# Kernel tuning notes

Hardware: AMD Instinct MI355X
Metric: run time of the kernel (lower is better)

## Reference

```python
import jax, jax.numpy as jnp
import numpy as np

# dims
T, INPUT_DIM = 128, 512
C_INT, ISQ, DIM, C = 8, 16, 256, 8  # internal_channels, input_square_dim, dim, n_channel
OSQ, OUT_CH = 8, 16                  # output_square_dim, output_size // osq^2
INPUT_SCALE, S1, S2 = 1.0, 0.9, 0.1
K1, D1, K2, D2 = 3, 1, 5, 2


def dw_circ_conv(x, w, dilation):
    """Depthwise conv with circular padding. x: [B,C,H,W], w: [C,1,k,k]."""
    k = w.shape[-1]
    pad = dilation * (k - 1) // 2
    xp = jnp.pad(x, ((0, 0), (0, 0), (pad, pad), (pad, pad)), mode='wrap')
    return jax.lax.conv_general_dilated(
        xp, w, window_strides=(1, 1), padding='VALID',
        rhs_dilation=(dilation, dilation), feature_group_count=x.shape[1])


def setup_inputs() -> dict:
    key = jax.random.key(0)
    ks = jax.random.split(key, 10)
    X = jax.random.normal(ks[0], (T, INPUT_DIM), jnp.float32)
    # nn.Linear weight [out, in]
    W_embed = jax.random.normal(ks[1], (C_INT * ISQ * ISQ, INPUT_DIM), jnp.float32) * 0.02
    mask_coarse = jax.random.bernoulli(ks[2], 0.5, (1, 1, ISQ, ISQ)).astype(jnp.float32)
    mask_fine = jax.random.bernoulli(ks[3], 0.5, (1, 1, DIM, DIM)).astype(jnp.float32)
    # ConvTranspose2d weight [in_ch, out_ch, k, k], k = dim // isq = 16
    W_deconv = jax.random.normal(ks[4], (C_INT, C, DIM // ISQ, DIM // ISQ), jnp.float32) * 0.02

    def lateral_w(k, ksz, p):
        # LateralConnections with conn_exp=1: |w| * bernoulli(p), normalized per output channel
        w = jnp.abs(jax.random.normal(k, (C, 1, ksz, ksz), jnp.float32))
        m = jax.random.bernoulli(jax.random.fold_in(k, 1), p, w.shape).astype(jnp.float32)
        w = w * m
        return w / w.sum(axis=(1, 2, 3), keepdims=True)

    w1 = lateral_w(ks[5], K1, 0.9)
    w2 = lateral_w(ks[6], K2, 0.9)
    # output Conv2d: [out_ch, in_ch, k, k], k = dim // osq = 32
    w_out = jax.random.normal(ks[7], (OUT_CH, C, DIM // OSQ, DIM // OSQ), jnp.float32) * 0.01
    b_out = jax.random.normal(ks[8], (OUT_CH,), jnp.float32) * 0.01
    return dict(X=X, W_embed=W_embed, mask_coarse=mask_coarse, mask_fine=mask_fine,
                W_deconv=W_deconv, w1=w1, w2=w2, w_out=w_out, b_out=b_out)


def reference(X, W_embed, mask_coarse, mask_fine, W_deconv, w1, w2, w_out, b_out):
    t = X.shape[0]
    ksz = W_deconv.shape[-1]
    # CorticalInput
    u = (X @ W_embed.T).reshape(t, C_INT, ISQ, ISQ) * mask_coarse  # [T,Cint,isq,isq]
    # ConvTranspose2d with stride == kernel_size (non-overlapping) == block expansion
    u = jnp.einsum('tcij,coab->toiajb', u, W_deconv).reshape(t, C, ISQ * ksz, ISQ * ksz)
    u = INPUT_SCALE * u * mask_fine  # [T,C,dim,dim]

    # sequential reservoir scan
    def step(Z, x):
        Z = jnp.tanh(S1 * dw_circ_conv(Z, w1, D1) + S2 * dw_circ_conv(Z, w2, D2) + x)
        return Z, Z[0]

    Z0 = jnp.zeros((1, C, DIM, DIM), X.dtype)
    _, outs = jax.lax.scan(step, Z0, u)  # outs: [T,C,dim,dim]

    # readout conv (kernel == stride == dim // osq)
    ko = w_out.shape[-1]
    y = jax.lax.conv_general_dilated(outs, w_out, (ko, ko), 'VALID')
    y = y + b_out[None, :, None, None]
    return y.reshape(t, -1)
```

## Files before the change

### kernel.cpp

```cpp
#include <hip/hip_runtime.h>
#include <math.h>

#define SB_OFF   0
#define E_OFF    1048576
#define YP_OFF   1310720

__device__ __forceinline__ float fast_tanh(float x) {
  x = fminf(fmaxf(x, -15.f), 15.f);
  float ex = __expf(2.f * x);
  return __fdividef(ex - 1.f, ex + 1.f);
}

template <int CTRL>
__device__ __forceinline__ float dpp_add(float v) {
  int x = __builtin_amdgcn_update_dpp(0, __float_as_int(v), CTRL, 0xF, 0xF, true);
  return v + __int_as_float(x);
}

__device__ __forceinline__ float2 aload_f2(const float* p) {
  unsigned long long v = __hip_atomic_load((const unsigned long long*)p,
                                           __ATOMIC_RELAXED, __HIP_MEMORY_SCOPE_AGENT);
  float2 r;
  r.x = __uint_as_float((unsigned)v);
  r.y = __uint_as_float((unsigned)(v >> 32));
  return r;
}
__device__ __forceinline__ void astore_f2(float* p, float a, float b) {
  unsigned long long v =
      ((unsigned long long)__float_as_uint(b) << 32) | (unsigned long long)__float_as_uint(a);
  __hip_atomic_store((unsigned long long*)p, v, __ATOMIC_RELAXED, __HIP_MEMORY_SCOPE_AGENT);
}

__global__ __launch_bounds__(256) void prep_kernel(
    const float* __restrict__ X, const float* __restrict__ W_embed,
    const float* __restrict__ mask_coarse, float* __restrict__ ws)
{
  const int tid = threadIdx.x, bid = blockIdx.x;
  float* eb = ws + E_OFF;
  const int o  = bid * 8 + (tid >> 5);
  const int t0 = (tid & 31) * 4;
  const float4* Wf4 = (const float4*)W_embed + (size_t)o * 128;
  const float4* Xf4 = (const float4*)X;
  float acc[4] = {0.f, 0.f, 0.f, 0.f};
  for (int k4 = 0; k4 < 128; ++k4) {
    float4 wv = Wf4[k4];
#pragma unroll
    for (int tt = 0; tt < 4; ++tt) {
      float4 xv = Xf4[(size_t)(t0 + tt) * 128 + k4];
      acc[tt] = fmaf(wv.x, xv.x, fmaf(wv.y, xv.y, fmaf(wv.z, xv.z, fmaf(wv.w, xv.w, acc[tt]))));
    }
  }
  float mc = mask_coarse[o & 255];
#pragma unroll
  for (int tt = 0; tt < 4; ++tt)
    eb[(size_t)(t0 + tt) * 2048 + o] = acc[tt] * mc;
}

__global__ __launch_bounds__(512, 2) void scan_kernel(
    const float* __restrict__ mask_fine, const float* __restrict__ W_deconv,
    const float* __restrict__ w1, const float* __restrict__ w2,
    const float* __restrict__ w_out, float* __restrict__ ws)
{
  __shared__ float zin[72 * 44];
  __shared__ float rowbuf[64 * 19];

  const int tid  = threadIdx.x;
  const int bid  = blockIdx.x;
  const int ch   = bid >> 5;
  const int tile = bid & 31;
  const int tI = tile >> 3, tJ = tile & 7;
  const int r0 = tI << 6, c0 = tJ << 5;
  const int row = tid >> 3;
  const int cg  = tid & 7;
  const int lc  = cg << 2;

  float* Zb = ws + SB_OFF;
  const float* eb = ws + E_OFF;
  float* yp = ws + YP_OFF;
  const int myoff = (ch * 32 + tile) << 11;

  const int a16 = row & 15;
  const int b16 = lc & 15;
  const int i0  = (r0 + row) >> 4;
  const int jj  = (c0 + lc) >> 4;
  float4 wd[8];
#pragma unroll
  for (int c = 0; c < 8; ++c)
    wd[c] = *(const float4*)&W_deconv[(((c * 8 + ch) * 16) + a16) * 16 + b16];
  float4 mf = *(const float4*)&mask_fine[(size_t)(r0 + row) * 256 + c0 + lc];
  float4 wo[16];
#pragma unroll
  for (int oc = 0; oc < 16; ++oc)
    wo[oc] = *(const float4*)&w_out[(((oc * 8 + ch) * 32) + (row & 31)) * 32 + lc];
  float w1s[9], w2s[25];
#pragma unroll
  for (int k = 0; k < 9; ++k)
    w1s[k] = __uint_as_float(__builtin_amdgcn_readfirstlane(__float_as_uint(w1[ch * 9 + k])));
#pragma unroll
  for (int k = 0; k < 25; ++k)
    w2s[k] = __uint_as_float(__builtin_amdgcn_readfirstlane(__float_as_uint(w2[ch * 25 + k])));

  int rd_off[2] = {0, 0}, rd_dst[2] = {0, 0};
  {
    int n = 0;
    auto setup = [&](int u) {
      int di = 0, dj = 0, off = 0, dst = 0;
      if (u < 128) {
        int r = u >> 5, c = u & 31;
        di = -1; dj = 0; off = 256 + 2 * u; dst = r * 44 + 4 + c;
      } else if (u < 256) {
        int v = u - 128;
        di = 1; dj = 0; off = 2 * v; dst = (68 + (v >> 5)) * 44 + 4 + (v & 31);
      } else if (u < 512) {
        int v = u - 256;
        di = 0; dj = -1; off = 1024 + 2 * v; dst = (4 + (v >> 2)) * 44 + (v & 3);
      } else if (u < 768) {
        int v = u - 512;
        di = 0; dj = 1; off = 512 + 2 * v; dst = (4 + (v >> 2)) * 44 + 36 + (v & 3);
      } else {
        int v = u - 768; int corner = v >> 4, k = v & 15, r = k >> 2, c = k & 3;
        if (corner == 0)      { di = -1; dj = -1; off = 1632 + 2 * k; dst = r * 44 + c; }
        else if (corner == 1) { di = -1; dj = 1;  off = 1600 + 2 * k; dst = r * 44 + 36 + c; }
        else if (corner == 2) { di = 1;  dj = -1; off = 1568 + 2 * k; dst = (68 + r) * 44 + c; }
        else                  { di = 1;  dj = 1;  off = 1536 + 2 * k; dst = (68 + r) * 44 + 36 + c; }
      }
      int nI = (tI + di) & 3, nJ = (tJ + dj) & 7;
      rd_off[n] = ((ch * 32 + nI * 8 + nJ) << 11) + off;
      rd_dst[n] = dst;
      ++n;
    };
    setup(tid);
    if (tid < 320) setup(tid + 512);
  }
  const bool has2 = (tid < 320);

  for (int k = tid; k < 72 * 44; k += 512) zin[k] = 0.f;
  __syncthreads();

  for (int t = 0; t < 128; ++t) {
    float* sb = Zb + (size_t)((t + 1) & 1) * 524288;

    float ev[8];
#pragma unroll
    for (int c = 0; c < 8; ++c)
      ev[c] = eb[(size_t)t * 2048 + c * 256 + i0 * 16 + jj];

    float c1a[4] = {0, 0, 0, 0}, c2a[4] = {0, 0, 0, 0};
    {
      float w[12];
      auto load_row = [&](int zr) {
        float4 A  = *(const float4*)&zin[zr * 44 + lc];
        float4 B  = *(const float4*)&zin[zr * 44 + lc + 4];
        float4 Cq = *(const float4*)&zin[zr * 44 + lc + 8];
        w[0]=A.x; w[1]=A.y; w[2]=A.z; w[3]=A.w;
        w[4]=B.x; w[5]=B.y; w[6]=B.z; w[7]=B.w;
        w[8]=Cq.x; w[9]=Cq.y; w[10]=Cq.z; w[11]=Cq.w;
      };
      auto k2row = [&](int a) {
#pragma unroll
        for (int j = 0; j < 4; ++j)
#pragma unroll
          for (int b = 0; b < 5; ++b)
            c2a[j] = fmaf(w[j + 2 * b], w2s[a * 5 + b], c2a[j]);
      };
      auto k1row = [&](int a) {
#pragma unroll
        for (int j = 0; j < 4; ++j)
#pragma unroll
          for (int b = 0; b < 3; ++b)
            c1a[j] = fmaf(w[j + 3 + b], w1s[a * 3 + b], c1a[j]);
      };
      load_row(row + 0); k2row(0);
      load_row(row + 2); k2row(1);
      load_row(row + 3); k1row(0);
      load_row(row + 4); k1row(1); k2row(2);
      load_row(row + 5); k1row(2);
      load_row(row + 6); k2row(3);
      load_row(row + 8); k2row(4);
    }
    float zv[4];
    {
      const float* mfp = (const float*)&mf;
#pragma unroll
      for (int j = 0; j < 4; ++j) {
        float u = 0.f;
#pragma unroll
        for (int c = 0; c < 8; ++c)
          u = fmaf(ev[c], ((const float*)&wd[c])[j], u);
        float val = fmaf(0.9f, c1a[j], fmaf(0.1f, c2a[j], mfp[j] * u));
        zv[j] = fast_tanh(val);
      }
    }

    if (t < 127) {
      float* myrec = sb + myoff;
      const float tagf = __uint_as_float((unsigned)(t + 1));
      if (row < 4) {
#pragma unroll
        for (int j = 0; j < 4; ++j)
          astore_f2(myrec + 2 * (row * 32 + lc + j), zv[j], tagf);
      }
      if (row >= 60) {
#pragma unroll
        for (int j = 0; j < 4; ++j)
          astore_f2(myrec + 256 + 2 * ((row - 60) * 32 + lc + j), zv[j], tagf);
      }
      if (lc == 0) {
#pragma unroll
        for (int j = 0; j < 4; ++j)
          astore_f2(myrec + 512 + 2 * (row * 4 + j), zv[j], tagf);
      }
      if (lc == 28) {
#pragma unroll
        for (int j = 0; j < 4; ++j)
          astore_f2(myrec + 1024 + 2 * (row * 4 + j), zv[j], tagf);
      }
      if (row < 4 && lc == 0) {
#pragma unroll
        for (int j = 0; j < 4; ++j)
          astore_f2(myrec + 1536 + 2 * (row * 4 + j), zv[j], tagf);
      }
      if (row < 4 && lc == 28) {
#pragma unroll
        for (int j = 0; j < 4; ++j)
          astore_f2(myrec + 1568 + 2 * (row * 4 + j), zv[j], tagf);
      }
      if (row >= 60 && lc == 0) {
#pragma unroll
        for (int j = 0; j < 4; ++j)
          astore_f2(myrec + 1600 + 2 * ((row - 60) * 4 + j), zv[j], tagf);
      }
      if (row >= 60 && lc == 28) {
#pragma unroll
        for (int j = 0; j < 4; ++j)
          astore_f2(myrec + 1632 + 2 * ((row - 60) * 4 + j), zv[j], tagf);
      }
    }

    float racc[16];
#pragma unroll
    for (int oc = 0; oc < 16; ++oc) {
      const float* wop = (const float*)&wo[oc];
      racc[oc] = fmaf(zv[0], wop[0], fmaf(zv[1], wop[1], fmaf(zv[2], wop[2], zv[3] * wop[3])));
    }

    __syncthreads();

    *(float4*)&zin[(4 + row) * 44 + 4 + lc] = make_float4(zv[0], zv[1], zv[2], zv[3]);

#pragma unroll
    for (int k = 0; k < 16; ++k) {
      racc[k] = dpp_add<0xB1>(racc[k]);
      racc[k] = dpp_add<0x4E>(racc[k]);
      racc[k] = dpp_add<0x141>(racc[k]);
    }
    rowbuf[row * 19 + (cg << 1)]     = racc[cg << 1];
    rowbuf[row * 19 + (cg << 1) + 1] = racc[(cg << 1) + 1];

    if (t < 127) {
      const unsigned tg = (unsigned)(t + 1);
      {
        const float* p = sb + rd_off[0];
        float2 v2; int spins = 0;
        do { v2 = aload_f2(p);
             if (__float_as_uint(v2.y) == tg) break;
             __builtin_amdgcn_s_sleep(1);
        } while (++spins < (1 << 17));
        zin[rd_dst[0]] = v2.x;
      }
      if (has2) {
        const float* p = sb + rd_off[1];
        float2 v2; int spins = 0;
        do { v2 = aload_f2(p);
             if (__float_as_uint(v2.y) == tg) break;
             __builtin_amdgcn_s_sleep(1);
        } while (++spins < (1 << 17));
        zin[rd_dst[1]] = v2.x;
      }
    }

    __syncthreads();

    if (tid < 32) {
      int p = tid >> 4, oc = tid & 15;
      float s = 0.f;
#pragma unroll
      for (int r = 0; r < 32; ++r) s += rowbuf[(p * 32 + r) * 19 + oc];
      yp[(((size_t)ch * 64 + (2 * tI + p) * 8 + tJ) * 128 + t) * 16 + oc] = s;
    }
  }
}

__global__ __launch_bounds__(256) void final_kernel(
    const float* __restrict__ b_out, const float* __restrict__ ws, float* __restrict__ out)
{
  int idx = blockIdx.x * 256 + threadIdx.x;
  int t = idx >> 10;
  int rem = idx & 1023;
  int oc = rem >> 6;
  int IJ = rem & 63;
  const float* yp = ws + YP_OFF;
  float s = b_out[oc];
#pragma unroll
  for (int c = 0; c < 8; ++c)
    s += yp[(((size_t)c * 64 + IJ) * 128 + t) * 16 + oc];
  out[idx] = s;
}

extern "C" void kernel_launch(void* const* d_in, const int* in_sizes, int n_in,
                              void* d_out, int out_size, void* d_ws, size_t ws_size,
                              hipStream_t stream) {
  const float* X           = (const float*)d_in[0];
  const float* W_embed     = (const float*)d_in[1];
  const float* mask_coarse = (const float*)d_in[2];
  const float* mask_fine   = (const float*)d_in[3];
  const float* W_deconv    = (const float*)d_in[4];
  const float* w1          = (const float*)d_in[5];
  const float* w2          = (const float*)d_in[6];
  const float* w_out       = (const float*)d_in[7];
  const float* b_out       = (const float*)d_in[8];
  float* ws  = (float*)d_ws;
  float* out = (float*)d_out;

  prep_kernel<<<dim3(256), dim3(256), 0, stream>>>(X, W_embed, mask_coarse, ws);
  scan_kernel<<<dim3(256), dim3(512), 0, stream>>>(mask_fine, W_deconv, w1, w2, w_out, ws);
  final_kernel<<<dim3(512), dim3(256), 0, stream>>>(b_out, ws, out);
}
```

Baseline: 555.8 us.

## Split scan into 512 smaller tiles and fuse readout reduction via atomics

Halves the spatial tile per block (32x32 instead of 64x32), doubling the grid to 512 blocks of 256 threads so more CUs take part in the sequential scan, with halo exchange records resized accordingly. The separate final reduction kernel is removed: prep initializes the output with the bias, and each scan block atomically adds its per-channel readout partial sums directly into the output. The smaller tiles mean more halo traffic per element and more inter-block spin synchronization. The atomic accumulation changes summation order, and all 512 blocks must be co-resident for the spin-wait scheme to work.

```diff
diff --git a/kernel.cpp b/kernel.cpp
--- a/kernel.cpp
+++ b/kernel.cpp
@@ -2,8 +2,7 @@
 #include <math.h>
 
 #define SB_OFF   0
-#define E_OFF    1048576
-#define YP_OFF   1310720
+#define E_OFF    1179648
 
 __device__ __forceinline__ float fast_tanh(float x) {
   x = fminf(fmaxf(x, -15.f), 15.f);
@@ -33,10 +32,18 @@
 
 __global__ __launch_bounds__(256) void prep_kernel(
     const float* __restrict__ X, const float* __restrict__ W_embed,
-    const float* __restrict__ mask_coarse, float* __restrict__ ws)
+    const float* __restrict__ mask_coarse, const float* __restrict__ b_out,
+    float* __restrict__ ws, float* __restrict__ out)
 {
   const int tid = threadIdx.x, bid = blockIdx.x;
   float* eb = ws + E_OFF;
+
+  {
+    int i0 = bid * 512 + tid * 2;
+    out[i0]     = b_out[(i0 >> 6) & 15];
+    out[i0 + 1] = b_out[((i0 + 1) >> 6) & 15];
+  }
+
   const int o  = bid * 8 + (tid >> 5);
   const int t0 = (tid & 31) * 4;
   const float4* Wf4 = (const float4*)W_embed + (size_t)o * 128;
@@ -56,30 +63,30 @@
     eb[(size_t)(t0 + tt) * 2048 + o] = acc[tt] * mc;
 }
 
-__global__ __launch_bounds__(512, 2) void scan_kernel(
+__global__ __launch_bounds__(256, 2) void scan_kernel(
     const float* __restrict__ mask_fine, const float* __restrict__ W_deconv,
     const float* __restrict__ w1, const float* __restrict__ w2,
-    const float* __restrict__ w_out, float* __restrict__ ws)
+    const float* __restrict__ w_out, float* __restrict__ ws,
+    float* __restrict__ out)
 {
-  __shared__ float zin[72 * 44];
-  __shared__ float rowbuf[64 * 19];
+  __shared__ float zin[40 * 44];
+  __shared__ float rowbuf[32 * 17];
 
   const int tid  = threadIdx.x;
   const int bid  = blockIdx.x;
-  const int ch   = bid >> 5;
-  const int tile = bid & 31;
+  const int ch   = bid >> 6;
+  const int tile = bid & 63;
   const int tI = tile >> 3, tJ = tile & 7;
-  const int r0 = tI << 6, c0 = tJ << 5;
+  const int r0 = tI << 5, c0 = tJ << 5;
   const int row = tid >> 3;
   const int cg  = tid & 7;
   const int lc  = cg << 2;
 
   float* Zb = ws + SB_OFF;
   const float* eb = ws + E_OFF;
-  float* yp = ws + YP_OFF;
-  const int myoff = (ch * 32 + tile) << 11;
-
-  const int a16 = row & 15;
+  const int myoff = (ch * 64 + tile) * 1152;
+
+  const int a16 = (r0 + row) & 15;
   const int b16 = lc & 15;
   const int i0  = (r0 + row) >> 4;
   const int jj  = (c0 + lc) >> 4;
@@ -91,7 +98,7 @@
   float4 wo[16];
 #pragma unroll
   for (int oc = 0; oc < 16; ++oc)
-    wo[oc] = *(const float4*)&w_out[(((oc * 8 + ch) * 32) + (row & 31)) * 32 + lc];
+    wo[oc] = *(const float4*)&w_out[(((oc * 8 + ch) * 32) + row) * 32 + lc];
   float w1s[9], w2s[25];
 #pragma unroll
   for (int k = 0; k < 9; ++k)
@@ -100,7 +107,7 @@
   for (int k = 0; k < 25; ++k)
     w2s[k] = __uint_as_float(__builtin_amdgcn_readfirstlane(__float_as_uint(w2[ch * 25 + k])));
 
-  int rd_off[2] = {0, 0}, rd_dst[2] = {0, 0};
+  int rd_off[3] = {0, 0, 0}, rd_dst[3] = {0, 0, 0};
   {
     int n = 0;
     auto setup = [&](int u) {
@@ -110,35 +117,36 @@
         di = -1; dj = 0; off = 256 + 2 * u; dst = r * 44 + 4 + c;
       } else if (u < 256) {
         int v = u - 128;
-        di = 1; dj = 0; off = 2 * v; dst = (68 + (v >> 5)) * 44 + 4 + (v & 31);
+        di = 1; dj = 0; off = 2 * v; dst = (36 + (v >> 5)) * 44 + 4 + (v & 31);
+      } else if (u < 384) {
+        int v = u - 256;
+        di = 0; dj = -1; off = 768 + 2 * v; dst = (4 + (v >> 2)) * 44 + (v & 3);
       } else if (u < 512) {
-        int v = u - 256;
-        di = 0; dj = -1; off = 1024 + 2 * v; dst = (4 + (v >> 2)) * 44 + (v & 3);
-      } else if (u < 768) {
-        int v = u - 512;
+        int v = u - 384;
         di = 0; dj = 1; off = 512 + 2 * v; dst = (4 + (v >> 2)) * 44 + 36 + (v & 3);
       } else {
-        int v = u - 768; int corner = v >> 4, k = v & 15, r = k >> 2, c = k & 3;
-        if (corner == 0)      { di = -1; dj = -1; off = 1632 + 2 * k; dst = r * 44 + c; }
-        else if (corner == 1) { di = -1; dj = 1;  off = 1600 + 2 * k; dst = r * 44 + 36 + c; }
-        else if (corner == 2) { di = 1;  dj = -1; off = 1568 + 2 * k; dst = (68 + r) * 44 + c; }
-        else                  { di = 1;  dj = 1;  off = 1536 + 2 * k; dst = (68 + r) * 44 + 36 + c; }
-      }
-      int nI = (tI + di) & 3, nJ = (tJ + dj) & 7;
-      rd_off[n] = ((ch * 32 + nI * 8 + nJ) << 11) + off;
+        int v = u - 512; int corner = v >> 4, k = v & 15, r = k >> 2, c = k & 3;
+        if (corner == 0)      { di = -1; dj = -1; off = 1120 + 2 * k; dst = r * 44 + c; }
+        else if (corner == 1) { di = -1; dj = 1;  off = 1088 + 2 * k; dst = r * 44 + 36 + c; }
+        else if (corner == 2) { di = 1;  dj = -1; off = 1056 + 2 * k; dst = (36 + r) * 44 + c; }
+        else                  { di = 1;  dj = 1;  off = 1024 + 2 * k; dst = (36 + r) * 44 + 36 + c; }
+      }
+      int nI = (tI + di) & 7, nJ = (tJ + dj) & 7;
+      rd_off[n] = (ch * 64 + nI * 8 + nJ) * 1152 + off;
       rd_dst[n] = dst;
       ++n;
     };
     setup(tid);
-    if (tid < 320) setup(tid + 512);
+    setup(tid + 256);
+    if (tid < 64) setup(tid + 512);
   }
-  const bool has2 = (tid < 320);
-
-  for (int k = tid; k < 72 * 44; k += 512) zin[k] = 0.f;
+  const bool has3 = (tid < 64);
+
+  for (int k = tid; k < 40 * 44; k += 256) zin[k] = 0.f;
   __syncthreads();
 
   for (int t = 0; t < 128; ++t) {
-    float* sb = Zb + (size_t)((t + 1) & 1) * 524288;
+    float* sb = Zb + (size_t)((t + 1) & 1) * 589824;
 
     float ev[8];
 #pragma unroll
@@ -200,10 +208,10 @@
         for (int j = 0; j < 4; ++j)
           astore_f2(myrec + 2 * (row * 32 + lc + j), zv[j], tagf);
       }
-      if (row >= 60) {
-#pragma unroll
-        for (int j = 0; j < 4; ++j)
-          astore_f2(myrec + 256 + 2 * ((row - 60) * 32 + lc + j), zv[j], tagf);
+      if (row >= 28) {
+#pragma unroll
+        for (int j = 0; j < 4; ++j)
+          astore_f2(myrec + 256 + 2 * ((row - 28) * 32 + lc + j), zv[j], tagf);
       }
       if (lc == 0) {
 #pragma unroll
@@ -213,27 +221,27 @@
       if (lc == 28) {
 #pragma unroll
         for (int j = 0; j < 4; ++j)
+          astore_f2(myrec + 768 + 2 * (row * 4 + j), zv[j], tagf);
+      }
+      if (row < 4 && lc == 0) {
+#pragma unroll
+        for (int j = 0; j < 4; ++j)
           astore_f2(myrec + 1024 + 2 * (row * 4 + j), zv[j], tagf);
       }
-      if (row < 4 && lc == 0) {
-#pragma unroll
-        for (int j = 0; j < 4; ++j)
-          astore_f2(myrec + 1536 + 2 * (row * 4 + j), zv[j], tagf);
-      }
       if (row < 4 && lc == 28) {
 #pragma unroll
         for (int j = 0; j < 4; ++j)
-          astore_f2(myrec + 1568 + 2 * (row * 4 + j), zv[j], tagf);
-      }
-      if (row >= 60 && lc == 0) {
-#pragma unroll
-        for (int j = 0; j < 4; ++j)
-          astore_f2(myrec + 1600 + 2 * ((row - 60) * 4 + j), zv[j], tagf);
-      }
-      if (row >= 60 && lc == 28) {
-#pragma unroll
-        for (int j = 0; j < 4; ++j)
-          astore_f2(myrec + 1632 + 2 * ((row - 60) * 4 + j), zv[j], tagf);
+          astore_f2(myrec + 1056 + 2 * (row * 4 + j), zv[j], tagf);
+      }
+      if (row >= 28 && lc == 0) {
+#pragma unroll
+        for (int j = 0; j < 4; ++j)
+          astore_f2(myrec + 1088 + 2 * ((row - 28) * 4 + j), zv[j], tagf);
+      }
+      if (row >= 28 && lc == 28) {
+#pragma unroll
+        for (int j = 0; j < 4; ++j)
+          astore_f2(myrec + 1120 + 2 * ((row - 28) * 4 + j), zv[j], tagf);
       }
     }
 
@@ -254,57 +262,41 @@
       racc[k] = dpp_add<0x4E>(racc[k]);
       racc[k] = dpp_add<0x141>(racc[k]);
     }
-    rowbuf[row * 19 + (cg << 1)]     = racc[cg << 1];
-    rowbuf[row * 19 + (cg << 1) + 1] = racc[(cg << 1) + 1];
+    rowbuf[row * 17 + (cg << 1)]     = racc[cg << 1];
+    rowbuf[row * 17 + (cg << 1) + 1] = racc[(cg << 1) + 1];
 
     if (t < 127) {
       const unsigned tg = (unsigned)(t + 1);
-      {
-        const float* p = sb + rd_off[0];
+#pragma unroll
+      for (int q = 0; q < 2; ++q) {
+        const float* p = sb + rd_off[q];
         float2 v2; int spins = 0;
         do { v2 = aload_f2(p);
              if (__float_as_uint(v2.y) == tg) break;
              __builtin_amdgcn_s_sleep(1);
-        } while (++spins < (1 << 17));
-        zin[rd_dst[0]] = v2.x;
-      }
-      if (has2) {
-        const float* p = sb + rd_off[1];
+        } while (++spins < (1 << 18));
+        zin[rd_dst[q]] = v2.x;
+      }
+      if (has3) {
+        const float* p = sb + rd_off[2];
         float2 v2; int spins = 0;
         do { v2 = aload_f2(p);
              if (__float_as_uint(v2.y) == tg) break;
              __builtin_amdgcn_s_sleep(1);
-        } while (++spins < (1 << 17));
-        zin[rd_dst[1]] = v2.x;
+        } while (++spins < (1 << 18));
+        zin[rd_dst[2]] = v2.x;
       }
     }
 
     __syncthreads();
 
-    if (tid < 32) {
-      int p = tid >> 4, oc = tid & 15;
+    if (tid < 16) {
       float s = 0.f;
 #pragma unroll
-      for (int r = 0; r < 32; ++r) s += rowbuf[(p * 32 + r) * 19 + oc];
-      yp[(((size_t)ch * 64 + (2 * tI + p) * 8 + tJ) * 128 + t) * 16 + oc] = s;
+      for (int r = 0; r < 32; ++r) s += rowbuf[r * 17 + tid];
+      atomicAdd(&out[t * 1024 + tid * 64 + tI * 8 + tJ], s);
     }
   }
-}
-
-__global__ __launch_bounds__(256) void final_kernel(
-    const float* __restrict__ b_out, const float* __restrict__ ws, float* __restrict__ out)
-{
-  int idx = blockIdx.x * 256 + threadIdx.x;
-  int t = idx >> 10;
-  int rem = idx & 1023;
-  int oc = rem >> 6;
-  int IJ = rem & 63;
-  const float* yp = ws + YP_OFF;
-  float s = b_out[oc];
-#pragma unroll
-  for (int c = 0; c < 8; ++c)
-    s += yp[(((size_t)c * 64 + IJ) * 128 + t) * 16 + oc];
-  out[idx] = s;
 }
 
 extern "C" void kernel_launch(void* const* d_in, const int* in_sizes, int n_in,
@@ -322,7 +314,6 @@
   float* ws  = (float*)d_ws;
   float* out = (float*)d_out;
 
-  prep_kernel<<<dim3(256), dim3(256), 0, stream>>>(X, W_embed, mask_coarse, ws);
-  scan_kernel<<<dim3(256), dim3(512), 0, stream>>>(mask_fine, W_deconv, w1, w2, w_out, ws);
-  final_kernel<<<dim3(512), dim3(256), 0, stream>>>(b_out, ws, out);
-}
+  prep_kernel<<<dim3(256), dim3(256), 0, stream>>>(X, W_embed, mask_coarse, b_out, ws, out);
+  scan_kernel<<<dim3(512), dim3(256), 0, stream>>>(mask_fine, W_deconv, w1, w2, w_out, ws, out);
+}
```

Result: slower. 633.0 us (+13.9%).

## Double-buffer halo/rowbuf shared memory, merge spin-waits, fuse readout via atomics

Applied to the files above, without the earlier changes.

Double-buffers the shared-memory tile and the row-reduction buffer so one of the two block barriers per timestep can be dropped. The two sequential halo spin-wait loops become a single loop that polls both flags at once. The final reduction kernel is removed: the prep kernel now writes the bias into the output and the scan kernel accumulates per-channel readout partials with atomicAdd. The prep GEMM is also regridded to twice as many blocks. The cost is doubled LDS use, atomic contention on the output, and a nondeterministic summation order.

```diff
diff --git a/kernel.cpp b/kernel.cpp
--- a/kernel.cpp
+++ b/kernel.cpp
@@ -3,7 +3,6 @@
 
 #define SB_OFF   0
 #define E_OFF    1048576
-#define YP_OFF   1310720
 
 __device__ __forceinline__ float fast_tanh(float x) {
   x = fminf(fmaxf(x, -15.f), 15.f);
@@ -33,36 +32,40 @@
 
 __global__ __launch_bounds__(256) void prep_kernel(
     const float* __restrict__ X, const float* __restrict__ W_embed,
-    const float* __restrict__ mask_coarse, float* __restrict__ ws)
+    const float* __restrict__ mask_coarse, const float* __restrict__ b_out,
+    float* __restrict__ ws, float* __restrict__ out)
 {
   const int tid = threadIdx.x, bid = blockIdx.x;
   float* eb = ws + E_OFF;
-  const int o  = bid * 8 + (tid >> 5);
-  const int t0 = (tid & 31) * 4;
+  {
+    int idx = bid * 256 + tid;
+    out[idx] = b_out[(idx >> 6) & 15];
+  }
+  const int o  = bid * 4 + (tid >> 6);
+  const int t0 = (tid & 63) * 2;
   const float4* Wf4 = (const float4*)W_embed + (size_t)o * 128;
   const float4* Xf4 = (const float4*)X;
-  float acc[4] = {0.f, 0.f, 0.f, 0.f};
+  float a0 = 0.f, a1 = 0.f;
   for (int k4 = 0; k4 < 128; ++k4) {
     float4 wv = Wf4[k4];
-#pragma unroll
-    for (int tt = 0; tt < 4; ++tt) {
-      float4 xv = Xf4[(size_t)(t0 + tt) * 128 + k4];
-      acc[tt] = fmaf(wv.x, xv.x, fmaf(wv.y, xv.y, fmaf(wv.z, xv.z, fmaf(wv.w, xv.w, acc[tt]))));
-    }
+    float4 x0 = Xf4[(size_t)t0 * 128 + k4];
+    float4 x1 = Xf4[(size_t)(t0 + 1) * 128 + k4];
+    a0 = fmaf(wv.x, x0.x, fmaf(wv.y, x0.y, fmaf(wv.z, x0.z, fmaf(wv.w, x0.w, a0))));
+    a1 = fmaf(wv.x, x1.x, fmaf(wv.y, x1.y, fmaf(wv.z, x1.z, fmaf(wv.w, x1.w, a1))));
   }
   float mc = mask_coarse[o & 255];
-#pragma unroll
-  for (int tt = 0; tt < 4; ++tt)
-    eb[(size_t)(t0 + tt) * 2048 + o] = acc[tt] * mc;
+  eb[(size_t)t0 * 2048 + o]       = a0 * mc;
+  eb[(size_t)(t0 + 1) * 2048 + o] = a1 * mc;
 }
 
 __global__ __launch_bounds__(512, 2) void scan_kernel(
     const float* __restrict__ mask_fine, const float* __restrict__ W_deconv,
     const float* __restrict__ w1, const float* __restrict__ w2,
-    const float* __restrict__ w_out, float* __restrict__ ws)
+    const float* __restrict__ w_out, float* __restrict__ ws,
+    float* __restrict__ out)
 {
-  __shared__ float zin[72 * 44];
-  __shared__ float rowbuf[64 * 19];
+  __shared__ float zin[2][72 * 44];
+  __shared__ float rowbuf[2][64 * 17];
 
   const int tid  = threadIdx.x;
   const int bid  = blockIdx.x;
@@ -76,17 +79,14 @@
 
   float* Zb = ws + SB_OFF;
   const float* eb = ws + E_OFF;
-  float* yp = ws + YP_OFF;
   const int myoff = (ch * 32 + tile) << 11;
 
-  const int a16 = row & 15;
-  const int b16 = lc & 15;
-  const int i0  = (r0 + row) >> 4;
-  const int jj  = (c0 + lc) >> 4;
+  const int i0 = (r0 + row) >> 4;
+  const int jj = (c0 + lc) >> 4;
   float4 wd[8];
 #pragma unroll
   for (int c = 0; c < 8; ++c)
-    wd[c] = *(const float4*)&W_deconv[(((c * 8 + ch) * 16) + a16) * 16 + b16];
+    wd[c] = *(const float4*)&W_deconv[(((c * 8 + ch) * 16) + (row & 15)) * 16 + (lc & 15)];
   float4 mf = *(const float4*)&mask_fine[(size_t)(r0 + row) * 256 + c0 + lc];
   float4 wo[16];
 #pragma unroll
@@ -134,11 +134,14 @@
   }
   const bool has2 = (tid < 320);
 
-  for (int k = tid; k < 72 * 44; k += 512) zin[k] = 0.f;
+  for (int k = tid; k < 2 * 72 * 44; k += 512) zin[0][k] = 0.f;
   __syncthreads();
 
   for (int t = 0; t < 128; ++t) {
     float* sb = Zb + (size_t)((t + 1) & 1) * 524288;
+    const float* zr = zin[t & 1];
+    float*       zw = zin[(t + 1) & 1];
+    float*       rb = rowbuf[t & 1];
 
     float ev[8];
 #pragma unroll
@@ -148,10 +151,10 @@
     float c1a[4] = {0, 0, 0, 0}, c2a[4] = {0, 0, 0, 0};
     {
       float w[12];
-      auto load_row = [&](int zr) {
-        float4 A  = *(const float4*)&zin[zr * 44 + lc];
-        float4 B  = *(const float4*)&zin[zr * 44 + lc + 4];
-        float4 Cq = *(const float4*)&zin[zr * 44 + lc + 8];
+      auto load_row = [&](int zrr) {
+        float4 A  = *(const float4*)&zr[zrr * 44 + lc];
+        float4 B  = *(const float4*)&zr[zrr * 44 + lc + 4];
+        float4 Cq = *(const float4*)&zr[zrr * 44 + lc + 8];
         w[0]=A.x; w[1]=A.y; w[2]=A.z; w[3]=A.w;
         w[4]=B.x; w[5]=B.y; w[6]=B.z; w[7]=B.w;
         w[8]=Cq.x; w[9]=Cq.y; w[10]=Cq.z; w[11]=Cq.w;
@@ -237,46 +240,38 @@
       }
     }
 
+    *(float4*)&zw[(4 + row) * 44 + 4 + lc] = make_float4(zv[0], zv[1], zv[2], zv[3]);
+
     float racc[16];
 #pragma unroll
     for (int oc = 0; oc < 16; ++oc) {
       const float* wop = (const float*)&wo[oc];
       racc[oc] = fmaf(zv[0], wop[0], fmaf(zv[1], wop[1], fmaf(zv[2], wop[2], zv[3] * wop[3])));
     }
-
-    __syncthreads();
-
-    *(float4*)&zin[(4 + row) * 44 + 4 + lc] = make_float4(zv[0], zv[1], zv[2], zv[3]);
-
 #pragma unroll
     for (int k = 0; k < 16; ++k) {
       racc[k] = dpp_add<0xB1>(racc[k]);
       racc[k] = dpp_add<0x4E>(racc[k]);
       racc[k] = dpp_add<0x141>(racc[k]);
     }
-    rowbuf[row * 19 + (cg << 1)]     = racc[cg << 1];
-    rowbuf[row * 19 + (cg << 1) + 1] = racc[(cg << 1) + 1];
+    rb[row * 17 + (cg << 1)]     = racc[cg << 1];
+    rb[row * 17 + (cg << 1) + 1] = racc[(cg << 1) + 1];
 
     if (t < 127) {
       const unsigned tg = (unsigned)(t + 1);
-      {
-        const float* p = sb + rd_off[0];
-        float2 v2; int spins = 0;
-        do { v2 = aload_f2(p);
-             if (__float_as_uint(v2.y) == tg) break;
-             __builtin_amdgcn_s_sleep(1);
-        } while (++spins < (1 << 17));
-        zin[rd_dst[0]] = v2.x;
-      }
-      if (has2) {
-        const float* p = sb + rd_off[1];
-        float2 v2; int spins = 0;
-        do { v2 = aload_f2(p);
-             if (__float_as_uint(v2.y) == tg) break;
-             __builtin_amdgcn_s_sleep(1);
-        } while (++spins < (1 << 17));
-        zin[rd_dst[1]] = v2.x;
-      }
+      const float* p0 = sb + rd_off[0];
+      const float* p1 = sb + rd_off[has2 ? 1 : 0];
+      float2 va = aload_f2(p0);
+      float2 vb = aload_f2(p1);
+      int spins = 0;
+      while ((__float_as_uint(va.y) != tg) || (__float_as_uint(vb.y) != tg)) {
+        if (++spins > (1 << 18)) break;
+        __builtin_amdgcn_s_sleep(1);
+        if (__float_as_uint(va.y) != tg) va = aload_f2(p0);
+        if (__float_as_uint(vb.y) != tg) vb = aload_f2(p1);
+      }
+      zw[rd_dst[0]] = va.x;
+      if (has2) zw[rd_dst[1]] = vb.x;
     }
 
     __syncthreads();
@@ -285,26 +280,10 @@
       int p = tid >> 4, oc = tid & 15;
       float s = 0.f;
 #pragma unroll
-      for (int r = 0; r < 32; ++r) s += rowbuf[(p * 32 + r) * 19 + oc];
-      yp[(((size_t)ch * 64 + (2 * tI + p) * 8 + tJ) * 128 + t) * 16 + oc] = s;
+      for (int r = 0; r < 32; ++r) s += rb[(p * 32 + r) * 17 + oc];
+      atomicAdd(&out[t * 1024 + oc * 64 + (2 * tI + p) * 8 + tJ], s);
     }
   }
-}
-
-__global__ __launch_bounds__(256) void final_kernel(
-    const float* __restrict__ b_out, const float* __restrict__ ws, float* __restrict__ out)
-{
-  int idx = blockIdx.x * 256 + threadIdx.x;
-  int t = idx >> 10;
-  int rem = idx & 1023;
-  int oc = rem >> 6;
-  int IJ = rem & 63;
-  const float* yp = ws + YP_OFF;
-  float s = b_out[oc];
-#pragma unroll
-  for (int c = 0; c < 8; ++c)
-    s += yp[(((size_t)c * 64 + IJ) * 128 + t) * 16 + oc];
-  out[idx] = s;
 }
 
 extern "C" void kernel_launch(void* const* d_in, const int* in_sizes, int n_in,
@@ -322,7 +301,6 @@
   float* ws  = (float*)d_ws;
   float* out = (float*)d_out;
 
-  prep_kernel<<<dim3(256), dim3(256), 0, stream>>>(X, W_embed, mask_coarse, ws);
-  scan_kernel<<<dim3(256), dim3(512), 0, stream>>>(mask_fine, W_deconv, w1, w2, w_out, ws);
-  final_kernel<<<dim3(512), dim3(256), 0, stream>>>(b_out, ws, out);
-}
+  prep_kernel<<<dim3(512), dim3(256), 0, stream>>>(X, W_embed, mask_coarse, b_out, ws, out);
+  scan_kernel<<<dim3(256), dim3(512), 0, stream>>>(mask_fine, W_deconv, w1, w2, w_out, ws, out);
+}
```

After: 573.7 us. +3.2%, slower.
